# Performance work log

Measured on AMD Instinct MI355X. Metric: run time of the kernel, lower is better.

Reference implementation:

```python
import jax, jax.numpy as jnp
import numpy as np

N, IN_DIM, OUT_DIM = 8192, 512, 512
ALPHA = 0.2  # leaky relu negative slope
NEG_BIG = -9e15

def _xavier(key, shape, gain=1.414):
    fan_in, fan_out = shape[0], shape[1]
    bound = gain * np.sqrt(6.0 / (fan_in + fan_out))
    return jax.random.uniform(key, shape, jnp.float32, -bound, bound)

def setup_inputs() -> dict:
    key = jax.random.key(0)
    k1, k2, k3, k4 = jax.random.split(key, 4)
    h = jax.random.normal(k1, (N, IN_DIM), jnp.float32)
    adj = jax.random.randint(k2, (N, N), 0, 2, jnp.int32)
    W = _xavier(k3, (IN_DIM, OUT_DIM))
    a = _xavier(k4, (2 * OUT_DIM, 1))
    return {"h": h, "adj": adj, "W": W, "a": a}

def reference(h, adj, W, a):
    Wh = h @ W                              # [N, out]
    # e_ij = leakyrelu(a1 . Wh_i + a2 . Wh_j) without the O(N^2*2d) concat
    a1 = a[:OUT_DIM, 0]                     # [out]
    a2 = a[OUT_DIM:, 0]                     # [out]
    f1 = Wh @ a1                            # [N]
    f2 = Wh @ a2                            # [N]
    e = jax.nn.leaky_relu(f1[:, None] + f2[None, :], negative_slope=ALPHA)
    e = jnp.where(adj > 0, e, NEG_BIG)
    attention = jax.nn.softmax(e, axis=1)   # dropout is identity in eval mode
    h_prime = attention @ Wh                # [N, out]
    return jax.nn.elu(h_prime)              # concat=True branch
```

## Files before the change

### kernel.cpp

```cpp
#include <hip/hip_runtime.h>
#include <stdint.h>

#define NN   8192
#define DIN  512
#define DOUT 512
#define ALPHA 0.2f

typedef float          floatx4  __attribute__((ext_vector_type(4)));
typedef float          floatx2  __attribute__((ext_vector_type(2)));
typedef short          shortx8  __attribute__((ext_vector_type(8)));
typedef unsigned short ushortx4 __attribute__((ext_vector_type(4)));
typedef int            intx2    __attribute__((ext_vector_type(2)));
typedef int            intx4    __attribute__((ext_vector_type(4)));
typedef unsigned       uintx2   __attribute__((ext_vector_type(2)));

__device__ inline unsigned short f2bf(float x) {
    union { float f; unsigned u; } v; v.f = x;
    return (unsigned short)((v.u + 0x7FFFu + ((v.u >> 16) & 1u)) >> 16);
}
__device__ inline unsigned encf(float x) {
    union { float f; unsigned u; } v; v.f = x;
    return (v.u & 0x80000000u) ? ~v.u : (v.u | 0x80000000u);
}
__device__ inline float decf(unsigned e) {
    union { float f; unsigned u; } v;
    v.u = (e & 0x80000000u) ? (e & 0x7FFFFFFFu) : ~e;
    return v.f;
}
__device__ inline float lrelu(float x) { return fmaxf(x, ALPHA * x); }

__global__ __launch_bounds__(256) void transpose_w(const float* __restrict__ W,
                                                   unsigned short* __restrict__ WT) {
    __shared__ float tile[32][33];
    const int t = threadIdx.x;
    const int x = t & 31, y = t >> 5;
    const int tr = (blockIdx.x >> 4) * 32, tc = (blockIdx.x & 15) * 32;
#pragma unroll
    for (int i = 0; i < 4; i++) {
        int r = y + i * 8;
        tile[r][x] = W[(size_t)(tr + r) * DOUT + tc + x];
    }
    __syncthreads();
#pragma unroll
    for (int i = 0; i < 4; i++) {
        int r = y + i * 8;
        WT[(size_t)(tc + r) * DIN + tr + x] = f2bf(tile[x][r]);
    }
}

__global__ __launch_bounds__(256) void gemm_wh(
    const float* __restrict__ h, const unsigned short* __restrict__ WT,
    const float* __restrict__ a, unsigned short* __restrict__ WhTt,
    float* __restrict__ f1, float* __restrict__ f2, unsigned* __restrict__ Menc)
{
    __shared__ float f1s[4][16], f2s[4][16];
    const int t = threadIdx.x;
    const int w = t >> 6, lane = t & 63, l15 = lane & 15, q = lane >> 4;
    const int r0 = blockIdx.x * 16;
    const int wc0 = w * 128;

    floatx4 acc[8];
    const floatx4 z4 = {0.f, 0.f, 0.f, 0.f};
#pragma unroll
    for (int j = 0; j < 8; j++) acc[j] = z4;

    const float* hp = &h[(size_t)(r0 + l15) * DIN + q * 8];
    const unsigned short* bp = &WT[(size_t)(wc0 + l15) * DIN + q * 8];

    floatx4 hA[2][2];
    shortx8 bB[2][8];
    hA[0][0] = *(const floatx4*)hp;
    hA[0][1] = *(const floatx4*)(hp + 4);
#pragma unroll
    for (int nt = 0; nt < 8; nt++)
        bB[0][nt] = *(const shortx8*)(bp + (size_t)nt * 16 * DIN);

#pragma unroll 2
    for (int it = 0; it < 16; ++it) {
        const int c = it & 1, n = c ^ 1;
        const int kn = ((it + 1) & 15) * 32;
        hA[n][0] = *(const floatx4*)(hp + kn);
        hA[n][1] = *(const floatx4*)(hp + kn + 4);
#pragma unroll
        for (int nt = 0; nt < 8; nt++)
            bB[n][nt] = *(const shortx8*)(bp + (size_t)nt * 16 * DIN + kn);

        shortx8 af;
#pragma unroll
        for (int j = 0; j < 8; j++)
            af[j] = (short)f2bf(hA[c][j >> 2][j & 3]);
#pragma unroll
        for (int nt = 0; nt < 8; nt++)
            acc[nt] = __builtin_amdgcn_mfma_f32_16x16x32_bf16(af, bB[c][nt], acc[nt], 0, 0, 0);
    }

    float a1v[8], a2v[8];
#pragma unroll
    for (int nt = 0; nt < 8; nt++) {
        int col = wc0 + nt * 16 + l15;
        a1v[nt] = a[col];
        a2v[nt] = a[DOUT + col];
    }
    {
        const int kk0 = r0 + q * 4;
        const int tile_k = kk0 >> 5;
        const int qq = (kk0 >> 3) & 3;
        const int j0 = kk0 & 7;
#pragma unroll
        for (int nt = 0; nt < 8; nt++) {
            const int tile_n = w * 8 + nt;
            ushortx4 pk;
#pragma unroll
            for (int reg = 0; reg < 4; reg++) pk[reg] = f2bf(acc[nt][reg]);
            *(ushortx4*)&WhTt[(((size_t)tile_k * 32 + tile_n) << 9) + qq * 128 + l15 * 8 + j0] = pk;
        }
    }
    float s1a[4], s2a[4];
#pragma unroll
    for (int reg = 0; reg < 4; reg++) {
        float s1 = 0.f, s2 = 0.f;
#pragma unroll
        for (int nt = 0; nt < 8; nt++) {
            s1 += acc[nt][reg] * a1v[nt];
            s2 += acc[nt][reg] * a2v[nt];
        }
        s1 += __shfl_xor(s1, 1, 64); s2 += __shfl_xor(s2, 1, 64);
        s1 += __shfl_xor(s1, 2, 64); s2 += __shfl_xor(s2, 2, 64);
        s1 += __shfl_xor(s1, 4, 64); s2 += __shfl_xor(s2, 4, 64);
        s1 += __shfl_xor(s1, 8, 64); s2 += __shfl_xor(s2, 8, 64);
        s1a[reg] = s1; s2a[reg] = s2;
    }
    if (l15 == 0) {
#pragma unroll
        for (int reg = 0; reg < 4; reg++) {
            f1s[w][q * 4 + reg] = s1a[reg];
            f2s[w][q * 4 + reg] = s2a[reg];
        }
    }
    __syncthreads();
    if (t < 16) {
        float v1 = f1s[0][t] + f1s[1][t] + f1s[2][t] + f1s[3][t];
        float v2 = f2s[0][t] + f2s[1][t] + f2s[2][t] + f2s[3][t];
        f1[r0 + t] = v1;
        f2[r0 + t] = v2;
        float mx = v2;
        mx = fmaxf(mx, __shfl_xor(mx, 1, 64));
        mx = fmaxf(mx, __shfl_xor(mx, 2, 64));
        mx = fmaxf(mx, __shfl_xor(mx, 4, 64));
        mx = fmaxf(mx, __shfl_xor(mx, 8, 64));
        if (t == 0) atomicMax(Menc, encf(mx));
    }
}

__global__ __launch_bounds__(1024, 4) void gat_agg(
    const int* __restrict__ adj, const unsigned short* __restrict__ WhTt,
    const float* __restrict__ f1, const float* __restrict__ f2,
    const unsigned* __restrict__ Menc, float* __restrict__ P,
    float* __restrict__ D)
{
    __shared__ __align__(16) unsigned short pbuf[2][128 * 40];
    __shared__ float f2s[2048];
    __shared__ float lsp[8][128];

    const int t = threadIdx.x;
    const int w = t >> 6, lane = t & 63, l15 = lane & 15, q = lane >> 4;
    const int prow = t >> 3, pk = t & 7;

    const int kq = blockIdx.x & 3;
    const int rgid = blockIdx.x >> 2;
    const int r0 = rgid * 128;
    const int k0 = kq * 2048;
    const int it0 = ((blockIdx.x >> 3) * 2) & 63;

    *(floatx2*)&f2s[t * 2] = *(const floatx2*)&f2[k0 + t * 2];

    const float M = decf(*Menc);
    const float f1v = f1[r0 + prow];
    const float mi = lrelu(f1v + M);

    floatx4 acc[8][2];
    const floatx4 z4 = {0.f, 0.f, 0.f, 0.f};
#pragma unroll
    for (int i = 0; i < 8; i++)
#pragma unroll
        for (int j = 0; j < 2; j++) acc[i][j] = z4;
    float ls = 0.f;

    const unsigned short* bpp = WhTt
        + (((size_t)(kq * 64) * 32 + w * 2) << 9) + lane * 8;
    const int* arp = adj + (size_t)(r0 + prow) * NN + k0 + pk * 4;

    intx4   adjr[2];
    floatx4 ffr[2];
    shortx8 breg[2][2];

    __syncthreads();

    {
        const int pA = it0, pB = (it0 + 1) & 63;
        adjr[0] = __builtin_nontemporal_load((const intx4*)(arp + pA * 32));
        adjr[1] = __builtin_nontemporal_load((const intx4*)(arp + pB * 32));
        ffr[0] = *(const floatx4*)&f2s[pA * 32 + pk * 4];
        ffr[1] = *(const floatx4*)&f2s[pB * 32 + pk * 4];
        float p0 = __expf(lrelu(f1v + ffr[0][0]) - mi);
        float p1 = __expf(lrelu(f1v + ffr[0][1]) - mi);
        float p2 = __expf(lrelu(f1v + ffr[0][2]) - mi);
        float p3 = __expf(lrelu(f1v + ffr[0][3]) - mi);
        p0 = (adjr[0][0] > 0) ? p0 : 0.f;
        p1 = (adjr[0][1] > 0) ? p1 : 0.f;
        p2 = (adjr[0][2] > 0) ? p2 : 0.f;
        p3 = (adjr[0][3] > 0) ? p3 : 0.f;
        ls += (p0 + p1) + (p2 + p3);
        uintx2 dd;
        dd[0] = __builtin_amdgcn_perm(__float_as_uint(p1), __float_as_uint(p0), 0x07060302u);
        dd[1] = __builtin_amdgcn_perm(__float_as_uint(p3), __float_as_uint(p2), 0x07060302u);
        *(uintx2*)&pbuf[0][prow * 40 + pk * 4] = dd;
        breg[0][0] = *(const shortx8*)(bpp + (size_t)pA * 16384);
        breg[0][1] = *(const shortx8*)(bpp + (size_t)pA * 16384 + 512);
    }
    __syncthreads();

#pragma unroll 2
    for (int it = 0; it < 64; ++it) {
        const int c = it & 1, n = c ^ 1;
        const int px1 = (it + 1 + it0) & 63;
        const int px2 = (it + 2 + it0) & 63;

        breg[n][0] = *(const shortx8*)(bpp + (size_t)px1 * 16384);
        breg[n][1] = *(const shortx8*)(bpp + (size_t)px1 * 16384 + 512);
        const intx4   ad_n = adjr[n];
        const floatx4 ff_n = ffr[n];
        adjr[c] = __builtin_nontemporal_load((const intx4*)(arp + px2 * 32));
        ffr[c] = *(const floatx4*)&f2s[px2 * 32 + pk * 4];

        if (it < 63) {
            float p0 = __expf(lrelu(f1v + ff_n[0]) - mi);
            float p1 = __expf(lrelu(f1v + ff_n[1]) - mi);
            float p2 = __expf(lrelu(f1v + ff_n[2]) - mi);
            float p3 = __expf(lrelu(f1v + ff_n[3]) - mi);
            p0 = (ad_n[0] > 0) ? p0 : 0.f;
            p1 = (ad_n[1] > 0) ? p1 : 0.f;
            p2 = (ad_n[2] > 0) ? p2 : 0.f;
            p3 = (ad_n[3] > 0) ? p3 : 0.f;
            ls += (p0 + p1) + (p2 + p3);
            uintx2 dd;
            dd[0] = __builtin_amdgcn_perm(__float_as_uint(p1), __float_as_uint(p0), 0x07060302u);
            dd[1] = __builtin_amdgcn_perm(__float_as_uint(p3), __float_as_uint(p2), 0x07060302u);
            *(uintx2*)&pbuf[n][prow * 40 + pk * 4] = dd;
        }

        __builtin_amdgcn_s_setprio(1);
#pragma unroll
        for (int rg = 0; rg < 8; rg++) {
            const shortx8 af = *(const shortx8*)&pbuf[c][(rg * 16 + l15) * 40 + q * 8];
            acc[rg][0] = __builtin_amdgcn_mfma_f32_16x16x32_bf16(af, breg[c][0], acc[rg][0], 0, 0, 0);
            acc[rg][1] = __builtin_amdgcn_mfma_f32_16x16x32_bf16(af, breg[c][1], acc[rg][1], 0, 0, 0);
        }
        __builtin_amdgcn_s_setprio(0);

        asm volatile("s_waitcnt lgkmcnt(0)" ::: "memory");
        __builtin_amdgcn_s_barrier();
    }

    lsp[pk][prow] = ls;
    __syncthreads();
    if (t < 128) {
        float s = 0.f;
#pragma unroll
        for (int kc = 0; kc < 8; kc++) s += lsp[kc][t];
        D[kq * NN + r0 + t] = s;
    }

    float* Pq = P + (size_t)kq * ((size_t)NN * DOUT) + (size_t)r0 * DOUT;
#pragma unroll
    for (int rg = 0; rg < 8; rg++)
#pragma unroll
        for (int nt = 0; nt < 2; nt++) {
            const int col = w * 32 + nt * 16 + l15;
#pragma unroll
            for (int reg = 0; reg < 4; reg++) {
                const int row = rg * 16 + q * 4 + reg;
                Pq[(size_t)row * DOUT + col] = acc[rg][nt][reg];
            }
        }
}

__global__ __launch_bounds__(1024) void gat_fin(
    const float* __restrict__ P, const float* __restrict__ D,
    float* __restrict__ out)
{
    const int t = threadIdx.x;
    const int r0 = blockIdx.x * 32;
    const int rr = t >> 7;
    const int c4 = (t & 127) * 4;
    const size_t Q = (size_t)NN * DOUT;
#pragma unroll
    for (int j = 0; j < 4; j++) {
        const int row = r0 + j * 8 + rr;
        const float den = ((D[row] + D[NN + row]) + (D[2 * NN + row] + D[3 * NN + row]));
        const float li = 1.f / den;
        const size_t off = (size_t)row * DOUT + c4;
        floatx4 v0 = *(const floatx4*)(P + off);
        floatx4 v1 = *(const floatx4*)(P + Q + off);
        floatx4 v2 = *(const floatx4*)(P + 2 * Q + off);
        floatx4 v3 = *(const floatx4*)(P + 3 * Q + off);
        floatx4 s;
#pragma unroll
        for (int i = 0; i < 4; i++) {
            float x = ((v0[i] + v1[i]) + (v2[i] + v3[i])) * li;
            s[i] = (x > 0.f) ? x : (__expf(x) - 1.f);
        }
        __builtin_nontemporal_store(s, (floatx4*)(out + off));
    }
}

extern "C" void kernel_launch(void* const* d_in, const int* in_sizes, int n_in,
                              void* d_out, int out_size, void* d_ws, size_t ws_size,
                              hipStream_t stream) {
    const float* h   = (const float*)d_in[0];
    const int*   adj = (const int*)d_in[1];
    const float* W   = (const float*)d_in[2];
    const float* a   = (const float*)d_in[3];
    float* out = (float*)d_out;

    char* ws = (char*)d_ws;
    unsigned short* WT    = (unsigned short*)ws;
    unsigned short* WhTt  = (unsigned short*)(ws + 524288);
    float*          f1    = (float*)(ws + 8912896);
    float*          f2    = (float*)(ws + 8945664);
    unsigned*       Menc  = (unsigned*)(ws + 8978432);
    float*          D     = (float*)(ws + 9437184);
    float*          P     = (float*)(ws + 16777216);

    hipMemsetAsync(Menc, 0, 4, stream);
    transpose_w<<<256, 256, 0, stream>>>(W, WT);
    gemm_wh<<<512, 256, 0, stream>>>(h, WT, a, WhTt, f1, f2, Menc);
    gat_agg<<<256, 1024, 0, stream>>>(adj, WhTt, f1, f2, Menc, P, D);
    gat_fin<<<256, 1024, 0, stream>>>(P, D, out);
}
```

Before: 454.1 us.

## Retile aggregation warps to 64x64 tiles and drop B-fragment prefetch and f2 LDS staging

Each of the 16 waves now computes a 64-row by 64-column output tile (2x8 wave grid) instead of all 128 rows by 32 columns, so each wave makes 4 A-fragment LDS reads per step instead of 8 and reuses each across 4 MFMAs. The WhT B fragments are no longer double-buffered one iteration ahead; four are loaded at the start of each iteration and used in the same iteration. The f2 values are read straight from global memory instead of being staged in LDS, which removes that shared array and the initial barrier. The aim is lower LDS traffic per MFMA. The cost is that B-load latency is now exposed within each iteration, and each block reads twice as much WhT data from L2.

```diff
diff --git a/kernel.cpp b/kernel.cpp
--- a/kernel.cpp
+++ b/kernel.cpp
@@ -159,12 +159,12 @@
     float* __restrict__ D)
 {
     __shared__ __align__(16) unsigned short pbuf[2][128 * 40];
-    __shared__ float f2s[2048];
     __shared__ float lsp[8][128];
 
     const int t = threadIdx.x;
     const int w = t >> 6, lane = t & 63, l15 = lane & 15, q = lane >> 4;
     const int prow = t >> 3, pk = t & 7;
+    const int rb = w >> 3, cw = w & 7;
 
     const int kq = blockIdx.x & 3;
     const int rgid = blockIdx.x >> 2;
@@ -172,36 +172,32 @@
     const int k0 = kq * 2048;
     const int it0 = ((blockIdx.x >> 3) * 2) & 63;
 
-    *(floatx2*)&f2s[t * 2] = *(const floatx2*)&f2[k0 + t * 2];
-
     const float M = decf(*Menc);
     const float f1v = f1[r0 + prow];
     const float mi = lrelu(f1v + M);
 
-    floatx4 acc[8][2];
+    floatx4 acc[4][4];
     const floatx4 z4 = {0.f, 0.f, 0.f, 0.f};
 #pragma unroll
-    for (int i = 0; i < 8; i++)
-#pragma unroll
-        for (int j = 0; j < 2; j++) acc[i][j] = z4;
+    for (int i = 0; i < 4; i++)
+#pragma unroll
+        for (int j = 0; j < 4; j++) acc[i][j] = z4;
     float ls = 0.f;
 
     const unsigned short* bpp = WhTt
-        + (((size_t)(kq * 64) * 32 + w * 2) << 9) + lane * 8;
+        + (((size_t)(kq * 64) * 32 + cw * 4) << 9) + lane * 8;
     const int* arp = adj + (size_t)(r0 + prow) * NN + k0 + pk * 4;
+    const float* f2p = f2 + k0 + pk * 4;
 
     intx4   adjr[2];
     floatx4 ffr[2];
-    shortx8 breg[2][2];
-
-    __syncthreads();
 
     {
         const int pA = it0, pB = (it0 + 1) & 63;
         adjr[0] = __builtin_nontemporal_load((const intx4*)(arp + pA * 32));
         adjr[1] = __builtin_nontemporal_load((const intx4*)(arp + pB * 32));
-        ffr[0] = *(const floatx4*)&f2s[pA * 32 + pk * 4];
-        ffr[1] = *(const floatx4*)&f2s[pB * 32 + pk * 4];
+        ffr[0] = *(const floatx4*)(f2p + pA * 32);
+        ffr[1] = *(const floatx4*)(f2p + pB * 32);
         float p0 = __expf(lrelu(f1v + ffr[0][0]) - mi);
         float p1 = __expf(lrelu(f1v + ffr[0][1]) - mi);
         float p2 = __expf(lrelu(f1v + ffr[0][2]) - mi);
@@ -215,23 +211,25 @@
         dd[0] = __builtin_amdgcn_perm(__float_as_uint(p1), __float_as_uint(p0), 0x07060302u);
         dd[1] = __builtin_amdgcn_perm(__float_as_uint(p3), __float_as_uint(p2), 0x07060302u);
         *(uintx2*)&pbuf[0][prow * 40 + pk * 4] = dd;
-        breg[0][0] = *(const shortx8*)(bpp + (size_t)pA * 16384);
-        breg[0][1] = *(const shortx8*)(bpp + (size_t)pA * 16384 + 512);
     }
     __syncthreads();
 
 #pragma unroll 2
     for (int it = 0; it < 64; ++it) {
         const int c = it & 1, n = c ^ 1;
-        const int px1 = (it + 1 + it0) & 63;
+        const int px0 = (it + it0) & 63;
         const int px2 = (it + 2 + it0) & 63;
 
-        breg[n][0] = *(const shortx8*)(bpp + (size_t)px1 * 16384);
-        breg[n][1] = *(const shortx8*)(bpp + (size_t)px1 * 16384 + 512);
+        const unsigned short* bq = bpp + (size_t)px0 * 16384;
+        shortx8 breg0 = *(const shortx8*)(bq);
+        shortx8 breg1 = *(const shortx8*)(bq + 512);
+        shortx8 breg2 = *(const shortx8*)(bq + 1024);
+        shortx8 breg3 = *(const shortx8*)(bq + 1536);
+
         const intx4   ad_n = adjr[n];
         const floatx4 ff_n = ffr[n];
         adjr[c] = __builtin_nontemporal_load((const intx4*)(arp + px2 * 32));
-        ffr[c] = *(const floatx4*)&f2s[px2 * 32 + pk * 4];
+        ffr[c] = *(const floatx4*)(f2p + px2 * 32);
 
         if (it < 63) {
             float p0 = __expf(lrelu(f1v + ff_n[0]) - mi);
@@ -251,10 +249,12 @@
 
         __builtin_amdgcn_s_setprio(1);
 #pragma unroll
-        for (int rg = 0; rg < 8; rg++) {
-            const shortx8 af = *(const shortx8*)&pbuf[c][(rg * 16 + l15) * 40 + q * 8];
-            acc[rg][0] = __builtin_amdgcn_mfma_f32_16x16x32_bf16(af, breg[c][0], acc[rg][0], 0, 0, 0);
-            acc[rg][1] = __builtin_amdgcn_mfma_f32_16x16x32_bf16(af, breg[c][1], acc[rg][1], 0, 0, 0);
+        for (int rg = 0; rg < 4; rg++) {
+            const shortx8 af = *(const shortx8*)&pbuf[c][(rb * 64 + rg * 16 + l15) * 40 + q * 8];
+            acc[rg][0] = __builtin_amdgcn_mfma_f32_16x16x32_bf16(af, breg0, acc[rg][0], 0, 0, 0);
+            acc[rg][1] = __builtin_amdgcn_mfma_f32_16x16x32_bf16(af, breg1, acc[rg][1], 0, 0, 0);
+            acc[rg][2] = __builtin_amdgcn_mfma_f32_16x16x32_bf16(af, breg2, acc[rg][2], 0, 0, 0);
+            acc[rg][3] = __builtin_amdgcn_mfma_f32_16x16x32_bf16(af, breg3, acc[rg][3], 0, 0, 0);
         }
         __builtin_amdgcn_s_setprio(0);
 
@@ -273,13 +273,13 @@
 
     float* Pq = P + (size_t)kq * ((size_t)NN * DOUT) + (size_t)r0 * DOUT;
 #pragma unroll
-    for (int rg = 0; rg < 8; rg++)
-#pragma unroll
-        for (int nt = 0; nt < 2; nt++) {
-            const int col = w * 32 + nt * 16 + l15;
+    for (int rg = 0; rg < 4; rg++)
+#pragma unroll
+        for (int nt = 0; nt < 4; nt++) {
+            const int col = cw * 64 + nt * 16 + l15;
 #pragma unroll
             for (int reg = 0; reg < 4; reg++) {
-                const int row = rg * 16 + q * 4 + reg;
+                const int row = rb * 64 + rg * 16 + q * 4 + reg;
                 Pq[(size_t)row * DOUT + col] = acc[rg][nt][reg];
             }
         }
```

Measured after the change: 470.1 us. +3.5%, slower.

## Batch four k-steps per barrier in GAT aggregation loop

Applied to the files above, without the earlier changes.

Restructures the aggregation main loop so each group computes four 32-wide probability tiles into LDS before a single barrier, then runs four MFMA steps over them, instead of one barrier per step. The goal is to cut the number of block-wide barriers by four and give the scheduler larger independent chunks to overlap. In exchange, LDS for pbuf grows fourfold (about 80KB with the double buffer), which may lower occupancy, and the adj prefetch for the next group is issued all at once.

```diff
diff --git a/kernel.cpp b/kernel.cpp
--- a/kernel.cpp
+++ b/kernel.cpp
@@ -158,7 +158,7 @@
     const unsigned* __restrict__ Menc, float* __restrict__ P,
     float* __restrict__ D)
 {
-    __shared__ __align__(16) unsigned short pbuf[2][128 * 40];
+    __shared__ __align__(16) unsigned short pbuf[2][4][128 * 40];
     __shared__ float f2s[2048];
     __shared__ float lsp[8][128];
 
@@ -170,7 +170,7 @@
     const int rgid = blockIdx.x >> 2;
     const int r0 = rgid * 128;
     const int k0 = kq * 2048;
-    const int it0 = ((blockIdx.x >> 3) * 2) & 63;
+    const int it0 = ((blockIdx.x >> 3) * 4) & 63;
 
     *(floatx2*)&f2s[t * 2] = *(const floatx2*)&f2[k0 + t * 2];
 
@@ -190,78 +190,71 @@
         + (((size_t)(kq * 64) * 32 + w * 2) << 9) + lane * 8;
     const int* arp = adj + (size_t)(r0 + prow) * NN + k0 + pk * 4;
 
-    intx4   adjr[2];
-    floatx4 ffr[2];
+    intx4   adjr[4];
     shortx8 breg[2][2];
 
     __syncthreads();
 
-    {
-        const int pA = it0, pB = (it0 + 1) & 63;
-        adjr[0] = __builtin_nontemporal_load((const intx4*)(arp + pA * 32));
-        adjr[1] = __builtin_nontemporal_load((const intx4*)(arp + pB * 32));
-        ffr[0] = *(const floatx4*)&f2s[pA * 32 + pk * 4];
-        ffr[1] = *(const floatx4*)&f2s[pB * 32 + pk * 4];
-        float p0 = __expf(lrelu(f1v + ffr[0][0]) - mi);
-        float p1 = __expf(lrelu(f1v + ffr[0][1]) - mi);
-        float p2 = __expf(lrelu(f1v + ffr[0][2]) - mi);
-        float p3 = __expf(lrelu(f1v + ffr[0][3]) - mi);
-        p0 = (adjr[0][0] > 0) ? p0 : 0.f;
-        p1 = (adjr[0][1] > 0) ? p1 : 0.f;
-        p2 = (adjr[0][2] > 0) ? p2 : 0.f;
-        p3 = (adjr[0][3] > 0) ? p3 : 0.f;
-        ls += (p0 + p1) + (p2 + p3);
-        uintx2 dd;
-        dd[0] = __builtin_amdgcn_perm(__float_as_uint(p1), __float_as_uint(p0), 0x07060302u);
-        dd[1] = __builtin_amdgcn_perm(__float_as_uint(p3), __float_as_uint(p2), 0x07060302u);
-        *(uintx2*)&pbuf[0][prow * 40 + pk * 4] = dd;
-        breg[0][0] = *(const shortx8*)(bpp + (size_t)pA * 16384);
-        breg[0][1] = *(const shortx8*)(bpp + (size_t)pA * 16384 + 512);
-    }
-    __syncthreads();
-
-#pragma unroll 2
-    for (int it = 0; it < 64; ++it) {
-        const int c = it & 1, n = c ^ 1;
-        const int px1 = (it + 1 + it0) & 63;
-        const int px2 = (it + 2 + it0) & 63;
-
-        breg[n][0] = *(const shortx8*)(bpp + (size_t)px1 * 16384);
-        breg[n][1] = *(const shortx8*)(bpp + (size_t)px1 * 16384 + 512);
-        const intx4   ad_n = adjr[n];
-        const floatx4 ff_n = ffr[n];
-        adjr[c] = __builtin_nontemporal_load((const intx4*)(arp + px2 * 32));
-        ffr[c] = *(const floatx4*)&f2s[px2 * 32 + pk * 4];
-
-        if (it < 63) {
-            float p0 = __expf(lrelu(f1v + ff_n[0]) - mi);
-            float p1 = __expf(lrelu(f1v + ff_n[1]) - mi);
-            float p2 = __expf(lrelu(f1v + ff_n[2]) - mi);
-            float p3 = __expf(lrelu(f1v + ff_n[3]) - mi);
-            p0 = (ad_n[0] > 0) ? p0 : 0.f;
-            p1 = (ad_n[1] > 0) ? p1 : 0.f;
-            p2 = (ad_n[2] > 0) ? p2 : 0.f;
-            p3 = (ad_n[3] > 0) ? p3 : 0.f;
+#pragma unroll
+    for (int j = 0; j < 4; j++)
+        adjr[j] = __builtin_nontemporal_load((const intx4*)(arp + ((it0 + j) & 63) * 32));
+    breg[0][0] = *(const shortx8*)(bpp + (size_t)it0 * 16384);
+    breg[0][1] = *(const shortx8*)(bpp + (size_t)it0 * 16384 + 512);
+
+#pragma unroll 1
+    for (int g = 0; g < 16; ++g) {
+        const int gb = g & 1;
+
+#pragma unroll
+        for (int j = 0; j < 4; j++) {
+            const int px = (g * 4 + j + it0) & 63;
+            const floatx4 ff = *(const floatx4*)&f2s[px * 32 + pk * 4];
+            const intx4   ad = adjr[j];
+            float p0 = __expf(lrelu(f1v + ff[0]) - mi);
+            float p1 = __expf(lrelu(f1v + ff[1]) - mi);
+            float p2 = __expf(lrelu(f1v + ff[2]) - mi);
+            float p3 = __expf(lrelu(f1v + ff[3]) - mi);
+            p0 = (ad[0] > 0) ? p0 : 0.f;
+            p1 = (ad[1] > 0) ? p1 : 0.f;
+            p2 = (ad[2] > 0) ? p2 : 0.f;
+            p3 = (ad[3] > 0) ? p3 : 0.f;
             ls += (p0 + p1) + (p2 + p3);
             uintx2 dd;
             dd[0] = __builtin_amdgcn_perm(__float_as_uint(p1), __float_as_uint(p0), 0x07060302u);
             dd[1] = __builtin_amdgcn_perm(__float_as_uint(p3), __float_as_uint(p2), 0x07060302u);
-            *(uintx2*)&pbuf[n][prow * 40 + pk * 4] = dd;
-        }
-
-        __builtin_amdgcn_s_setprio(1);
-#pragma unroll
-        for (int rg = 0; rg < 8; rg++) {
-            const shortx8 af = *(const shortx8*)&pbuf[c][(rg * 16 + l15) * 40 + q * 8];
-            acc[rg][0] = __builtin_amdgcn_mfma_f32_16x16x32_bf16(af, breg[c][0], acc[rg][0], 0, 0, 0);
-            acc[rg][1] = __builtin_amdgcn_mfma_f32_16x16x32_bf16(af, breg[c][1], acc[rg][1], 0, 0, 0);
-        }
-        __builtin_amdgcn_s_setprio(0);
+            *(uintx2*)&pbuf[gb][j][prow * 40 + pk * 4] = dd;
+        }
+
+        {
+            const int gn = (g + 1) & 15;
+#pragma unroll
+            for (int j = 0; j < 4; j++)
+                adjr[j] = __builtin_nontemporal_load(
+                    (const intx4*)(arp + ((gn * 4 + j + it0) & 63) * 32));
+        }
 
         asm volatile("s_waitcnt lgkmcnt(0)" ::: "memory");
         __builtin_amdgcn_s_barrier();
-    }
-
+
+#pragma unroll
+        for (int j = 0; j < 4; j++) {
+            const int c = (g * 4 + j) & 1, n = c ^ 1;
+            const int pxn = (g * 4 + j + 1 + it0) & 63;
+            breg[n][0] = *(const shortx8*)(bpp + (size_t)pxn * 16384);
+            breg[n][1] = *(const shortx8*)(bpp + (size_t)pxn * 16384 + 512);
+
+            __builtin_amdgcn_s_setprio(1);
+#pragma unroll
+            for (int rg = 0; rg < 8; rg++) {
+                const shortx8 af = *(const shortx8*)&pbuf[gb][j][(rg * 16 + l15) * 40 + q * 8];
+                acc[rg][0] = __builtin_amdgcn_mfma_f32_16x16x32_bf16(af, breg[c][0], acc[rg][0], 0, 0, 0);
+                acc[rg][1] = __builtin_amdgcn_mfma_f32_16x16x32_bf16(af, breg[c][1], acc[rg][1], 0, 0, 0);
+            }
+            __builtin_amdgcn_s_setprio(0);
+        }
+    }
+
+    __syncthreads();
     lsp[pk][prow] = ls;
     __syncthreads();
     if (t < 128) {
```

After: 432.8 us (median of 2 runs). -4.7%, faster.
